# Performance work log

Hardware: AMD Instinct MI355X
Metric: run time of the kernel (lower is better)

## Reference

```python
import jax, jax.numpy as jnp
import numpy as np

THRESHOLD = 33.33  # torch forward default

def setup_inputs() -> dict:
    key = jax.random.key(0)
    k1, k2 = jax.random.split(key)
    source_pc = jax.random.normal(k1, (2, 16384, 3), dtype=jnp.float32)
    target_pc = jax.random.normal(k2, (2, 16384, 3), dtype=jnp.float32)
    return {"source_pc": source_pc, "target_pc": target_pc}

def _pairwise_dist(x, y):
    # Euclidean cdist via the matmul expansion (same math as torch.cdist p=2).
    # x: [B, N, D], y: [B, M, D] -> [B, N, M]
    x2 = jnp.sum(x * x, axis=-1)              # [B, N]
    y2 = jnp.sum(y * y, axis=-1)              # [B, M]
    xy = jnp.einsum('bnd,bmd->bnm', x, y)     # [B, N, M]
    d2 = x2[:, :, None] + y2[None if False else slice(None), None, :] - 2.0 * xy
    d2 = x2[:, :, None] + y2[:, None, :] - 2.0 * xy
    return jnp.sqrt(jnp.maximum(d2, 0.0))

def reference(source_pc, target_pc):
    dist = _pairwise_dist(source_pc.astype(jnp.float32), target_pc.astype(jnp.float32))
    dist1 = jnp.minimum(jnp.min(dist, axis=2), THRESHOLD)  # [B, N] clamped
    dist2 = jnp.minimum(jnp.min(dist, axis=1), THRESHOLD)  # [B, M] clamped
    d1 = jnp.mean(dist1, axis=-1)
    d2 = jnp.mean(dist2, axis=-1)
    return (d1 + d2) / 2.0  # bidirectional=True default -> [B]
```

## Files before the change

kernel.cpp:

```cpp
#include <hip/hip_runtime.h>

#define NPTS 16384
#define TH 33.33f

typedef __attribute__((ext_vector_type(8)))  __bf16 bf16x8;
typedef __attribute__((ext_vector_type(16))) float  f32x16;
typedef __attribute__((ext_vector_type(16))) unsigned u32x16;

__device__ __forceinline__ unsigned short f2bf(float x) {
    unsigned u = __float_as_uint(x);
    u += 0x7FFFu + ((u >> 16) & 1u);
    return (unsigned short)(u >> 16);
}
__device__ __forceinline__ float bf2f(unsigned short h) {
    return __uint_as_float(((unsigned)h) << 16);
}
__device__ __forceinline__ unsigned umin_(unsigned a, unsigned b) { return a < b ? a : b; }

union UV { uint4 v; bf16x8 h; unsigned short s[8]; };


__global__ __launch_bounds__(256) void prep_kernel(
        const float* __restrict__ src, const float* __restrict__ tgt,
        unsigned char* __restrict__ pfmt, float* __restrict__ out)
{
    const int set = blockIdx.y;
    const int chunk = blockIdx.x;
    const int tid = threadIdx.x;
    if (set == 0 && chunk == 0 && tid < 2) out[tid] = 0.0f;
    const float* base = (set < 2 ? src : tgt) + (size_t)(set & 1) * NPTS * 3;
    const int p = chunk * 256 + tid;
    const float x = base[p * 3 + 0], y = base[p * 3 + 1], z = base[p * 3 + 2];

    float hp = 0.5f * fmaf(z, z, fmaf(y, y, x * x));
    unsigned short xh = f2bf(x), yh = f2bf(y), zh = f2bf(z);
    unsigned short xl = f2bf(x - bf2f(xh)), yl = f2bf(y - bf2f(yh)), zl = f2bf(z - bf2f(zh));
    float rr = hp;
    unsigned short h0 = f2bf(rr); rr -= bf2f(h0);
    unsigned short h1 = f2bf(rr); rr -= bf2f(h1);
    unsigned short h2 = f2bf(rr);
    UV c0, c1;
    c0.s[0]=xh; c0.s[1]=yh; c0.s[2]=zh; c0.s[3]=xh; c0.s[4]=yh; c0.s[5]=zh; c0.s[6]=xl; c0.s[7]=yl;
    c1.s[0]=zl; c1.s[1]=(unsigned short)(h0^0x8000); c1.s[2]=(unsigned short)(h1^0x8000);
    c1.s[3]=(unsigned short)(h2^0x8000);
    c1.s[4]=0xC200;
    c1.s[5]=0; c1.s[6]=0; c1.s[7]=0;

    unsigned char* ob = pfmt + (size_t)set * NPTS * 32
                             + (size_t)(p >> 5) * 1024 + (size_t)(p & 31) * 16;
    *(uint4*)(ob)       = c0.v;
    *(uint4*)(ob + 512) = c1.v;
}

__global__ __launch_bounds__(256, 8) void chamfer_kernel(
        const float* __restrict__ src, const float* __restrict__ tgt,
        const unsigned char* __restrict__ pfmt, float* __restrict__ d2part)
{
    const int db = blockIdx.y, dir = db >> 1, b = db & 1;
    const int rowblock = blockIdx.x >> 3, seg = blockIdx.x & 7;
    const int tid = threadIdx.x, wave = tid >> 6, lane = tid & 63;
    const int g = lane >> 5, cc = lane & 31;
    const float* qp = (dir == 0 ? src : tgt) + (size_t)b * NPTS * 3;
    const int pset = (dir == 0 ? 2 + b : b);
    const unsigned char* ps = pfmt + (size_t)pset * NPTS * 32 + (size_t)seg * 2048 * 32;
    const unsigned short one = 0x3F80;

    __shared__ alignas(16) unsigned char smem[16896];
    unsigned* scratch = (unsigned*)smem;

    const int rt = rowblock * 4 + wave;
    bf16x8 afrag; float hq;
    {
        int r = rt * 32 + cc;
        float x = qp[r * 3 + 0], y = qp[r * 3 + 1], z = qp[r * 3 + 2];
        hq = 0.5f * fmaf(z, z, fmaf(y, y, x * x));
        unsigned short xh = f2bf(x), yh = f2bf(y), zh = f2bf(z);
        unsigned short xl = f2bf(x - bf2f(xh)), yl = f2bf(y - bf2f(yh)), zl = f2bf(z - bf2f(zh));
        UV f0, f1, rv;
        f0.s[0]=xh; f0.s[1]=yh; f0.s[2]=zh; f0.s[3]=xl; f0.s[4]=yl; f0.s[5]=zl; f0.s[6]=xh; f0.s[7]=yh;
        f1.s[0]=zh; f1.s[1]=one; f1.s[2]=one; f1.s[3]=one;
        f1.s[4]=one;
        f1.s[5]=0; f1.s[6]=0; f1.s[7]=0;
        rv.v = g ? f1.v : f0.v;
        afrag = rv.h;
    }

    u32x16 m0 = 0xFF800000u;
    const f32x16 zc = 0.0f;

    const unsigned char* gq = ps + (size_t)lane * 16;
#pragma unroll 1
    for (int i = 0; i < 32; ++i) {
        UV u0, u1;
        u0.v = *(const uint4*)(gq + (size_t)i * 2048);
        u1.v = *(const uint4*)(gq + (size_t)i * 2048 + 1024);
        f32x16 t0 = __builtin_amdgcn_mfma_f32_32x32x16_bf16(afrag, u0.h, zc, 0, 0, 0);
        f32x16 t1 = __builtin_amdgcn_mfma_f32_32x32x16_bf16(afrag, u1.h, zc, 0, 0, 0);
#pragma unroll
        for (int j = 0; j < 16; j++)
            m0[j] = umin_(umin_(__float_as_uint(t0[j]), __float_as_uint(t1[j])), m0[j]);
    }

    float* dst = d2part + (((size_t)(db * 128 + rowblock)) * 8 + seg) * 128;
    {
        unsigned* sc = scratch + wave * 1056;
#pragma unroll
        for (int j = 0; j < 16; j++) {
            int r0 = (j & 3) + 8 * (j >> 2) + 4 * g;
            sc[r0 * 33 + cc] = m0[j];
        }
        const unsigned* sr = sc + cc * 33 + g * 16;
        unsigned mx = 0xFF800000u;
#pragma unroll
        for (int k = 0; k < 16; k++) mx = umin_(mx, sr[k]);
        mx = umin_(mx, (unsigned)__shfl_xor((int)mx, 32, 64));
        if (lane < 32) {
            float sbi = __uint_as_float(mx);
            float d2 = 2.0f * (hq - 32.0f - sbi);
            float d = fminf(sqrtf(fmaxf(d2, 0.0f)), TH);
            dst[wave * 32 + lane] = d;
        }
    }
}

__global__ __launch_bounds__(256) void merge_kernel(const float* __restrict__ d2part,
                                                    float* __restrict__ out) {
    const int b = blockIdx.y;
    const int slice = blockIdx.x;
    const int tid = threadIdx.x;
    float s = 0.0f;
#pragma unroll
    for (int pass = 0; pass < 2; pass++) {
        const float* base = d2part + (size_t)(pass * 2 + b) * 128 * 8 * 128;
#pragma unroll
        for (int i = 0; i < 4; i++) {
            int r = slice * 1024 + i * 256 + tid;
            const float* p = base + (size_t)(r >> 7) * 1024 + (r & 127);
            float m = p[0];
#pragma unroll
            for (int sgi = 1; sgi < 8; sgi++) m = fminf(m, p[sgi * 128]);
            s += m;
        }
    }
#pragma unroll
    for (int off = 32; off > 0; off >>= 1) s += __shfl_down(s, off, 64);
    __shared__ float w[4];
    if ((tid & 63) == 0) w[tid >> 6] = s;
    __syncthreads();
    if (tid == 0) {
        float t = (w[0] + w[1]) + (w[2] + w[3]);
        atomicAdd(&out[b], t * (1.0f / (2.0f * NPTS)));
    }
}

extern "C" void kernel_launch(void* const* d_in, const int* in_sizes, int n_in,
                              void* d_out, int out_size, void* d_ws, size_t ws_size,
                              hipStream_t stream) {
    const float* src = (const float*)d_in[0];
    const float* tgt = (const float*)d_in[1];
    float* out = (float*)d_out;
    unsigned char* pfmt = (unsigned char*)d_ws;
    float* d2part = (float*)(pfmt + (size_t)4 * 1024 * 1024);

    prep_kernel<<<dim3(64, 4), 256, 0, stream>>>(src, tgt, pfmt, out);
    chamfer_kernel<<<dim3(1024, 4), 256, 0, stream>>>(src, tgt, pfmt, d2part);
    merge_kernel<<<dim3(16, 2), 256, 0, stream>>>(d2part, out);
}
```

Measured before the change: 96.32 us.

## Register-block four query tiles per wave and double-buffer target fragment loads

After: 91.27 us. -5.2%, faster.

```diff
diff --git a/kernel.cpp b/kernel.cpp
--- a/kernel.cpp
+++ b/kernel.cpp
@@ -52,7 +52,40 @@
     *(uint4*)(ob + 512) = c1.v;
 }
 
-__global__ __launch_bounds__(256, 8) void chamfer_kernel(
+#define BODY(Q0, Q1) { \
+    f32x16 t0, t1; \
+    t0 = __builtin_amdgcn_mfma_f32_32x32x16_bf16(af0, Q0, zc, 0, 0, 0); \
+    t1 = __builtin_amdgcn_mfma_f32_32x32x16_bf16(af0, Q1, zc, 0, 0, 0); \
+    _Pragma("unroll") for (int j = 0; j < 16; j++) \
+        mm0[j] = umin_(umin_(__float_as_uint(t0[j]), __float_as_uint(t1[j])), mm0[j]); \
+    t0 = __builtin_amdgcn_mfma_f32_32x32x16_bf16(af1, Q0, zc, 0, 0, 0); \
+    t1 = __builtin_amdgcn_mfma_f32_32x32x16_bf16(af1, Q1, zc, 0, 0, 0); \
+    _Pragma("unroll") for (int j = 0; j < 16; j++) \
+        mm1[j] = umin_(umin_(__float_as_uint(t0[j]), __float_as_uint(t1[j])), mm1[j]); \
+    t0 = __builtin_amdgcn_mfma_f32_32x32x16_bf16(af2, Q0, zc, 0, 0, 0); \
+    t1 = __builtin_amdgcn_mfma_f32_32x32x16_bf16(af2, Q1, zc, 0, 0, 0); \
+    _Pragma("unroll") for (int j = 0; j < 16; j++) \
+        mm2[j] = umin_(umin_(__float_as_uint(t0[j]), __float_as_uint(t1[j])), mm2[j]); \
+    t0 = __builtin_amdgcn_mfma_f32_32x32x16_bf16(af3, Q0, zc, 0, 0, 0); \
+    t1 = __builtin_amdgcn_mfma_f32_32x32x16_bf16(af3, Q1, zc, 0, 0, 0); \
+    _Pragma("unroll") for (int j = 0; j < 16; j++) \
+        mm3[j] = umin_(umin_(__float_as_uint(t0[j]), __float_as_uint(t1[j])), mm3[j]); }
+
+#define EPILOG(MM, P) { \
+    unsigned* sc = scratch + wave * 1056; \
+    _Pragma("unroll") for (int j = 0; j < 16; j++) { \
+        int r0 = (j & 3) + 8 * (j >> 2) + 4 * g; sc[r0 * 33 + cc] = MM[j]; } \
+    const unsigned* sr = sc + cc * 33 + g * 16; \
+    unsigned mx = 0xFF800000u; \
+    _Pragma("unroll") for (int k = 0; k < 16; k++) mx = umin_(mx, sr[k]); \
+    mx = umin_(mx, (unsigned)__shfl_xor((int)mx, 32, 64)); \
+    if (lane < 32) { \
+        float sbi = __uint_as_float(mx); \
+        float d2 = 2.0f * (hq[P] - 32.0f - sbi); \
+        float d = fminf(sqrtf(fmaxf(d2, 0.0f)), TH); \
+        dst[wave * 128 + (P) * 32 + lane] = d; } }
+
+__global__ __launch_bounds__(256, 2) void chamfer_kernel(
         const float* __restrict__ src, const float* __restrict__ tgt,
         const unsigned char* __restrict__ pfmt, float* __restrict__ d2part)
 {
@@ -68,12 +101,12 @@
     __shared__ alignas(16) unsigned char smem[16896];
     unsigned* scratch = (unsigned*)smem;
 
-    const int rt = rowblock * 4 + wave;
-    bf16x8 afrag; float hq;
-    {
-        int r = rt * 32 + cc;
+    bf16x8 af0, af1, af2, af3; float hq[4];
+#pragma unroll
+    for (int i = 0; i < 4; i++) {
+        int r = (rowblock * 16 + wave * 4 + i) * 32 + cc;
         float x = qp[r * 3 + 0], y = qp[r * 3 + 1], z = qp[r * 3 + 2];
-        hq = 0.5f * fmaf(z, z, fmaf(y, y, x * x));
+        hq[i] = 0.5f * fmaf(z, z, fmaf(y, y, x * x));
         unsigned short xh = f2bf(x), yh = f2bf(y), zh = f2bf(z);
         unsigned short xl = f2bf(x - bf2f(xh)), yl = f2bf(y - bf2f(yh)), zl = f2bf(z - bf2f(zh));
         UV f0, f1, rv;
@@ -82,45 +115,34 @@
         f1.s[4]=one;
         f1.s[5]=0; f1.s[6]=0; f1.s[7]=0;
         rv.v = g ? f1.v : f0.v;
-        afrag = rv.h;
+        if (i == 0) af0 = rv.h; else if (i == 1) af1 = rv.h;
+        else if (i == 2) af2 = rv.h; else af3 = rv.h;
     }
 
-    u32x16 m0 = 0xFF800000u;
+    u32x16 mm0 = 0xFF800000u, mm1 = 0xFF800000u, mm2 = 0xFF800000u, mm3 = 0xFF800000u;
     const f32x16 zc = 0.0f;
 
     const unsigned char* gq = ps + (size_t)lane * 16;
+    UV a0, a1, b0, b1;
+    a0.v = *(const uint4*)(gq);
+    a1.v = *(const uint4*)(gq + 1024);
 #pragma unroll 1
-    for (int i = 0; i < 32; ++i) {
-        UV u0, u1;
-        u0.v = *(const uint4*)(gq + (size_t)i * 2048);
-        u1.v = *(const uint4*)(gq + (size_t)i * 2048 + 1024);
-        f32x16 t0 = __builtin_amdgcn_mfma_f32_32x32x16_bf16(afrag, u0.h, zc, 0, 0, 0);
-        f32x16 t1 = __builtin_amdgcn_mfma_f32_32x32x16_bf16(afrag, u1.h, zc, 0, 0, 0);
-#pragma unroll
-        for (int j = 0; j < 16; j++)
-            m0[j] = umin_(umin_(__float_as_uint(t0[j]), __float_as_uint(t1[j])), m0[j]);
+    for (int i = 0; i < 32; i += 2) {
+        b0.v = *(const uint4*)(gq + (size_t)(i + 1) * 2048);
+        b1.v = *(const uint4*)(gq + (size_t)(i + 1) * 2048 + 1024);
+        BODY(a0.h, a1.h)
+        if (i + 2 < 32) {
+            a0.v = *(const uint4*)(gq + (size_t)(i + 2) * 2048);
+            a1.v = *(const uint4*)(gq + (size_t)(i + 2) * 2048 + 1024);
+        }
+        BODY(b0.h, b1.h)
     }
 
-    float* dst = d2part + (((size_t)(db * 128 + rowblock)) * 8 + seg) * 128;
-    {
-        unsigned* sc = scratch + wave * 1056;
-#pragma unroll
-        for (int j = 0; j < 16; j++) {
-            int r0 = (j & 3) + 8 * (j >> 2) + 4 * g;
-            sc[r0 * 33 + cc] = m0[j];
-        }
-        const unsigned* sr = sc + cc * 33 + g * 16;
-        unsigned mx = 0xFF800000u;
-#pragma unroll
-        for (int k = 0; k < 16; k++) mx = umin_(mx, sr[k]);
-        mx = umin_(mx, (unsigned)__shfl_xor((int)mx, 32, 64));
-        if (lane < 32) {
-            float sbi = __uint_as_float(mx);
-            float d2 = 2.0f * (hq - 32.0f - sbi);
-            float d = fminf(sqrtf(fmaxf(d2, 0.0f)), TH);
-            dst[wave * 32 + lane] = d;
-        }
-    }
+    float* dst = d2part + (((size_t)(db * 32 + rowblock)) * 8 + seg) * 512;
+    EPILOG(mm0, 0)
+    EPILOG(mm1, 1)
+    EPILOG(mm2, 2)
+    EPILOG(mm3, 3)
 }
 
 __global__ __launch_bounds__(256) void merge_kernel(const float* __restrict__ d2part,
@@ -131,14 +153,14 @@
     float s = 0.0f;
 #pragma unroll
     for (int pass = 0; pass < 2; pass++) {
-        const float* base = d2part + (size_t)(pass * 2 + b) * 128 * 8 * 128;
+        const float* base = d2part + (size_t)(pass * 2 + b) * 32 * 8 * 512;
 #pragma unroll
         for (int i = 0; i < 4; i++) {
             int r = slice * 1024 + i * 256 + tid;
-            const float* p = base + (size_t)(r >> 7) * 1024 + (r & 127);
+            const float* p = base + (size_t)(r >> 9) * 4096 + (r & 511);
             float m = p[0];
 #pragma unroll
-            for (int sgi = 1; sgi < 8; sgi++) m = fminf(m, p[sgi * 128]);
+            for (int sgi = 1; sgi < 8; sgi++) m = fminf(m, p[sgi * 512]);
             s += m;
         }
     }
@@ -163,6 +185,6 @@
     float* d2part = (float*)(pfmt + (size_t)4 * 1024 * 1024);
 
     prep_kernel<<<dim3(64, 4), 256, 0, stream>>>(src, tgt, pfmt, out);
-    chamfer_kernel<<<dim3(1024, 4), 256, 0, stream>>>(src, tgt, pfmt, d2part);
+    chamfer_kernel<<<dim3(256, 4), 256, 0, stream>>>(src, tgt, pfmt, d2part);
     merge_kernel<<<dim3(16, 2), 256, 0, stream>>>(d2part, out);
 }
```
